# Performance work log

Hardware: AMD Instinct MI355X
Metric: run time of the kernel (lower is better)

Reference implementation:

```python
import jax, jax.numpy as jnp
import numpy as np

TR = 14.7e-3
NT = 144
TAU = 1.8
T0 = TAU
T1B = 1.65
FA_PARAMS = (3.0, 12.0)
B = 262144


def _build_buffers():
    # t = arange(Nt)*TR + t0
    t = np.arange(NT, dtype=np.float64) * TR + T0
    # QUADRATIC flip-angle schedule: all t >= t0, so N = Nt
    n = NT
    alpha = FA_PARAMS[0] + (FA_PARAMS[1] - FA_PARAMS[0]) * (np.arange(n) / (n - 1)) ** 2
    # Attenuation recursion: R[0]=1, R[i]=R[i-1]*cos(deg2rad(alpha[i-1])) for t[i]>t0
    R = np.concatenate([[1.0], np.cumprod(np.cos(np.deg2rad(alpha[:-1])))])
    return (t.astype(np.float32), alpha.astype(np.float32), R.astype(np.float32))


def setup_inputs() -> dict:
    key = jax.random.key(0)
    x = jax.random.uniform(key, (B, 4), dtype=jnp.float32)  # [delta_t, s, p, amp]
    t, alpha, R = _build_buffers()
    return {"x": x, "t": jnp.asarray(t), "alpha": jnp.asarray(alpha), "R": jnp.asarray(R)}


def _togammainc(X, A):
    # scipy clamps negatives to 0 in both args, then regularized lower incomplete gamma P(A, X)
    X = jnp.maximum(X, 0.0)
    A = jnp.broadcast_to(jnp.maximum(A, 0.0), X.shape)
    return jax.scipy.special.gammainc(A, X)


def reference(x, t, alpha, R):
    delta_t = x[:, 0:1]  # [B,1]
    s = x[:, 1:2]
    p = x[:, 2:3]
    amp = x[:, 3:4]

    a = 1.0 + p * s                     # [B,1]
    sprime = s + 1.0 / T1B              # [B,1]
    SF = 2.0 * jnp.exp(-delta_t / T1B) * (s / sprime) ** a  # [B,1]

    td = t[None, :] - delta_t           # [B,Nt]
    G = _togammainc(sprime * td, a) - _togammainc(sprime * (td - TAU), a)  # [B,Nt]
    E = jnp.sin(jnp.deg2rad(alpha))     # [Nt]

    S = SF * R[None, :] * G * E[None, :]  # [B,Nt]
    return amp * S
```

## Files before the change

### kernel.cpp

```cpp
#include <hip/hip_runtime.h>
#include <cmath>

#define NT 144

typedef float v2f __attribute__((ext_vector_type(2)));


__global__ __launch_bounds__(256, 4) void dynangio_kernel(
    const float* __restrict__ x,
    const float* __restrict__ t,
    const float* __restrict__ alpha,
    const float* __restrict__ R,
    float* __restrict__ out,
    int B)
{
    __shared__ alignas(16) float sh_t[NT];
    __shared__ alignas(16) float sh_re[NT];
    const int tid = threadIdx.x;
    if (tid < NT) {
        sh_t[tid]  = t[tid];
        sh_re[tid] = R[tid] * sinf(alpha[tid] * 0.017453292519943295f);
    }
    __syncthreads();

    const int c   = tid & 3;
    const int row = blockIdx.x * 64 + (tid >> 2);
    if (row >= B) return;

    const float4 xi = reinterpret_cast<const float4*>(x)[row];
    const float dt  = xi.x;
    const float s   = xi.y;
    const float p   = xi.z;
    const float amp = xi.w;

    const float T1B   = 1.65f;
    const float TAU   = 1.8f;
    const float LOG2E = 1.4426950408889634f;

    const float u  = p * s;
    const float a  = 1.0f + u;
    const float sp = s + (1.0f / T1B);

    float g = 0.035868343f;
    g = g * u - 0.193527818f;
    g = g * u + 0.482199394f;
    g = g * u - 0.756704078f;
    g = g * u + 0.918206857f;
    g = g * u - 0.897056937f;
    g = g * u + 0.988205891f;
    g = g * u - 0.577191652f;
    g = g * u + 1.0f;
    const float Ga1 = (1.0f + u) * g;

    const float d18 = a + 18.0f;
    const float d17 = (a + 17.0f) * d18;
    const float d16 = (a + 16.0f) * d17;
    const float d15 = (a + 15.0f) * d16;
    const float d14 = (a + 14.0f) * d15;
    const float d13 = (a + 13.0f) * d14;
    const float d12 = (a + 12.0f) * d13;
    const float d11 = (a + 11.0f) * d12;
    const float d10 = (a + 10.0f) * d11;
    const float d9  = (a +  9.0f) * d10;
    const float d8  = (a +  8.0f) * d9;
    const float d7  = (a +  7.0f) * d8;
    const float d6  = (a +  6.0f) * d7;
    const float d5  = (a +  5.0f) * d6;
    const float d4  = (a +  4.0f) * d5;
    const float d3  = (a +  3.0f) * d4;
    const float d2  = (a +  2.0f) * d3;
    const float d1  = (a +  1.0f) * d2;

    const float invDG = 1.0f / (d1 * Ga1);

    const float SF = 2.0f * __builtin_amdgcn_exp2f(
        a * (__builtin_amdgcn_logf(s) - __builtin_amdgcn_logf(sp))
        - dt * (LOG2E / T1B));

    const float crow  = amp * SF * invDG;
    const float nspdt = -sp * dt;
    const float spTau = sp * TAU;
    v2f dtv; dtv.x = nspdt; dtv.y = nspdt - spTau;

    auto elem = [&](float tj, float cr) -> float {
        v2f tv; tv.x = tj; tv.y = tj;
        v2f X = sp * tv + dtv;
        X.y = fmaxf(X.y, 0.0f);
        const v2f Z = X * X;
        v2f NE = Z + d17;
        NE = Z*NE + d15;  NE = Z*NE + d13;  NE = Z*NE + d11;
        NE = Z*NE + d9;   NE = Z*NE + d7;   NE = Z*NE + d5;
        NE = Z*NE + d3;   NE = Z*NE + d1;
        v2f NO = Z*d18 + d16;
        NO = Z*NO + d14;  NO = Z*NO + d12;  NO = Z*NO + d10;
        NO = Z*NO + d8;   NO = Z*NO + d6;   NO = Z*NO + d4;
        NO = Z*NO + d2;
        const v2f N = X*NO + NE;
        v2f L; L.x = __builtin_amdgcn_logf(X.x); L.y = __builtin_amdgcn_logf(X.y);
        const v2f Ee = a * L - X * LOG2E;
        const float e1 = __builtin_amdgcn_exp2f(Ee.x);
        const float e2 = __builtin_amdgcn_exp2f(Ee.y);
        return cr * __builtin_fmaf(N.x, e1, -(N.y * e2));
    };

    float4* __restrict__ orow4 = reinterpret_cast<float4*>(out + (size_t)row * NT);
    const float4* sh_t4  = reinterpret_cast<const float4*>(sh_t);
    const float4* sh_re4 = reinterpret_cast<const float4*>(sh_re);

    #pragma unroll 1
    for (int k = 0; k < 9; ++k) {
        const int ch = c + 4 * k;
        const float4 tj4 = sh_t4[ch];
        const float4 re4 = sh_re4[ch];
        float4 res;
        res.x = elem(tj4.x, crow * re4.x);
        res.y = elem(tj4.y, crow * re4.y);
        res.z = elem(tj4.z, crow * re4.z);
        res.w = elem(tj4.w, crow * re4.w);
        orow4[ch] = res;
    }
}

extern "C" void kernel_launch(void* const* d_in, const int* in_sizes, int n_in,
                              void* d_out, int out_size, void* d_ws, size_t ws_size,
                              hipStream_t stream) {
    const float* x     = (const float*)d_in[0];
    const float* t     = (const float*)d_in[1];
    const float* alpha = (const float*)d_in[2];
    const float* R     = (const float*)d_in[3];
    float* out = (float*)d_out;

    const int B = in_sizes[0] / 4;
    const int rows_per_block = 64;
    const int blocks = (B + rows_per_block - 1) / rows_per_block;
    hipLaunchKernelGGL(dynangio_kernel, dim3(blocks), dim3(256), 0, stream,
                       x, t, alpha, R, out, B);
}
```

Before: 177.1 us.

## Use scalar Horner polynomial, prefetch shared loads, and nontemporal stores

Replaces the packed v2f even/odd-split polynomial with a single scalar Horner chain per argument, interleaving the two evaluations. Shared-memory t and R·sin(alpha) vectors are prefetched one iteration ahead so LDS latency overlaps the math. Output stores become nontemporal to avoid polluting cache. The plain Horner form uses fewer operations than the even/odd split but has a longer dependency chain and loses packed-FMA throughput.

```diff
diff --git a/kernel.cpp b/kernel.cpp
--- a/kernel.cpp
+++ b/kernel.cpp
@@ -3,7 +3,7 @@
 
 #define NT 144
 
-typedef float v2f __attribute__((ext_vector_type(2)));
+typedef float v4f __attribute__((ext_vector_type(4)));
 
 
 __global__ __launch_bounds__(256, 4) void dynangio_kernel(
@@ -80,44 +80,59 @@
     const float crow  = amp * SF * invDG;
     const float nspdt = -sp * dt;
     const float spTau = sp * TAU;
-    v2f dtv; dtv.x = nspdt; dtv.y = nspdt - spTau;
 
     auto elem = [&](float tj, float cr) -> float {
-        v2f tv; tv.x = tj; tv.y = tj;
-        v2f X = sp * tv + dtv;
-        X.y = fmaxf(X.y, 0.0f);
-        const v2f Z = X * X;
-        v2f NE = Z + d17;
-        NE = Z*NE + d15;  NE = Z*NE + d13;  NE = Z*NE + d11;
-        NE = Z*NE + d9;   NE = Z*NE + d7;   NE = Z*NE + d5;
-        NE = Z*NE + d3;   NE = Z*NE + d1;
-        v2f NO = Z*d18 + d16;
-        NO = Z*NO + d14;  NO = Z*NO + d12;  NO = Z*NO + d10;
-        NO = Z*NO + d8;   NO = Z*NO + d6;   NO = Z*NO + d4;
-        NO = Z*NO + d2;
-        const v2f N = X*NO + NE;
-        v2f L; L.x = __builtin_amdgcn_logf(X.x); L.y = __builtin_amdgcn_logf(X.y);
-        const v2f Ee = a * L - X * LOG2E;
-        const float e1 = __builtin_amdgcn_exp2f(Ee.x);
-        const float e2 = __builtin_amdgcn_exp2f(Ee.y);
-        return cr * __builtin_fmaf(N.x, e1, -(N.y * e2));
+        const float x1 = __builtin_fmaf(sp, tj, nspdt);
+        const float x2 = fmaxf(x1 - spTau, 0.0f);
+        const float l1 = __builtin_amdgcn_logf(x1);
+        const float l2 = __builtin_amdgcn_logf(x2);
+        float n1 = x1 + d18;
+        float n2 = x2 + d18;
+        n1 = __builtin_fmaf(n1, x1, d17);  n2 = __builtin_fmaf(n2, x2, d17);
+        n1 = __builtin_fmaf(n1, x1, d16);  n2 = __builtin_fmaf(n2, x2, d16);
+        n1 = __builtin_fmaf(n1, x1, d15);  n2 = __builtin_fmaf(n2, x2, d15);
+        n1 = __builtin_fmaf(n1, x1, d14);  n2 = __builtin_fmaf(n2, x2, d14);
+        n1 = __builtin_fmaf(n1, x1, d13);  n2 = __builtin_fmaf(n2, x2, d13);
+        n1 = __builtin_fmaf(n1, x1, d12);  n2 = __builtin_fmaf(n2, x2, d12);
+        n1 = __builtin_fmaf(n1, x1, d11);  n2 = __builtin_fmaf(n2, x2, d11);
+        n1 = __builtin_fmaf(n1, x1, d10);  n2 = __builtin_fmaf(n2, x2, d10);
+        n1 = __builtin_fmaf(n1, x1, d9);   n2 = __builtin_fmaf(n2, x2, d9);
+        n1 = __builtin_fmaf(n1, x1, d8);   n2 = __builtin_fmaf(n2, x2, d8);
+        n1 = __builtin_fmaf(n1, x1, d7);   n2 = __builtin_fmaf(n2, x2, d7);
+        n1 = __builtin_fmaf(n1, x1, d6);   n2 = __builtin_fmaf(n2, x2, d6);
+        n1 = __builtin_fmaf(n1, x1, d5);   n2 = __builtin_fmaf(n2, x2, d5);
+        n1 = __builtin_fmaf(n1, x1, d4);   n2 = __builtin_fmaf(n2, x2, d4);
+        n1 = __builtin_fmaf(n1, x1, d3);   n2 = __builtin_fmaf(n2, x2, d3);
+        n1 = __builtin_fmaf(n1, x1, d2);   n2 = __builtin_fmaf(n2, x2, d2);
+        n1 = __builtin_fmaf(n1, x1, d1);   n2 = __builtin_fmaf(n2, x2, d1);
+        const float e1 = __builtin_amdgcn_exp2f(
+            __builtin_fmaf(a, l1, -(x1 * LOG2E)));
+        const float e2 = __builtin_amdgcn_exp2f(
+            __builtin_fmaf(a, l2, -(x2 * LOG2E)));
+        return cr * __builtin_fmaf(n1, e1, -(n2 * e2));
     };
 
-    float4* __restrict__ orow4 = reinterpret_cast<float4*>(out + (size_t)row * NT);
-    const float4* sh_t4  = reinterpret_cast<const float4*>(sh_t);
-    const float4* sh_re4 = reinterpret_cast<const float4*>(sh_re);
+    v4f* __restrict__ orow4 = reinterpret_cast<v4f*>(out + (size_t)row * NT);
+    const v4f* sh_t4  = reinterpret_cast<const v4f*>(sh_t);
+    const v4f* sh_re4 = reinterpret_cast<const v4f*>(sh_re);
+
+    v4f tj4 = sh_t4[c];
+    v4f re4 = sh_re4[c];
 
     #pragma unroll 1
     for (int k = 0; k < 9; ++k) {
-        const int ch = c + 4 * k;
-        const float4 tj4 = sh_t4[ch];
-        const float4 re4 = sh_re4[ch];
-        float4 res;
+        const int ch  = c + 4 * k;
+        const int chn = (k < 8) ? ch + 4 : ch;
+        const v4f tj4n = sh_t4[chn];
+        const v4f re4n = sh_re4[chn];
+        v4f res;
         res.x = elem(tj4.x, crow * re4.x);
         res.y = elem(tj4.y, crow * re4.y);
         res.z = elem(tj4.z, crow * re4.z);
         res.w = elem(tj4.w, crow * re4.w);
-        orow4[ch] = res;
+        __builtin_nontemporal_store(res, &orow4[ch]);
+        tj4 = tj4n;
+        re4 = re4n;
     }
 }
 
```

Result: no change. 179.6 us (+1.4%).
